# Kernel optimization log

Measured on AMD Instinct MI355X. Metric: run time of the kernel, lower is better.

Reference implementation:

```python
import jax, jax.numpy as jnp
import numpy as np

N, E, D_IN, L, H, U = 20000, 320000, 256, 4, 4, 64
HID = H * U  # 256
OUT = 64
LN_EPS = 1e-3  # keras LayerNormalization default epsilon
NEG_SLOPE = 0.2


def layer_norm(x, g, b):
    m = jnp.mean(x, axis=-1, keepdims=True)
    v = jnp.var(x, axis=-1, keepdims=True)
    return (x - m) * jax.lax.rsqrt(v + LN_EPS) * g + b


def gatv2(x, dst, src, Wl, Wr, a):
    # x: [N, HID]; Wl/Wr: [HID, H, U]; a: [H, U]
    zl = jnp.einsum('nd,dhu->nhu', x, Wl)  # target projection
    zr = jnp.einsum('nd,dhu->nhu', x, Wr)  # source projection / messages
    f = jax.nn.leaky_relu(zl[dst] + zr[src], NEG_SLOPE)       # [E, H, U]
    s = jnp.einsum('ehu,hu->eh', f, a)                        # [E, H]
    smax = jax.ops.segment_max(s, dst, num_segments=N)        # [N, H]
    es = jnp.exp(s - smax[dst])
    denom = jax.ops.segment_sum(es, dst, num_segments=N)      # [N, H]
    agg = jax.ops.segment_sum(es[:, :, None] * zr[src], dst, num_segments=N)
    agg = agg / (denom[:, :, None] + 1e-9)                    # [N, H, U]
    return agg.reshape(N, HID) + x  # residual (input dim == H*U)


def setup_inputs() -> dict:
    key = jax.random.key(0)
    ks = jax.random.split(key, 10)
    s_in = 1.0 / np.sqrt(D_IN)
    s_h = 1.0 / np.sqrt(HID)
    return {
        'x': jax.random.normal(ks[0], (N, D_IN), jnp.float32),
        'head_W': jax.random.normal(ks[1], (D_IN, HID), jnp.float32) * s_in,
        'head_b': jnp.zeros((HID,), jnp.float32),
        'ng_g': jnp.ones((L, HID), jnp.float32),
        'ng_b': jnp.zeros((L, HID), jnp.float32),
        'Wl': jax.random.normal(ks[2], (L, HID, H, U), jnp.float32) * s_h,
        'Wr': jax.random.normal(ks[3], (L, HID, H, U), jnp.float32) * s_h,
        'att': jax.random.normal(ks[4], (L, H, U), jnp.float32) * (1.0 / np.sqrt(U)),
        'nd_g': jnp.ones((L, HID), jnp.float32),
        'nd_b': jnp.zeros((L, HID), jnp.float32),
        'dense_W': jax.random.normal(ks[5], (L, HID, 4 * HID), jnp.float32) * s_h,
        'dense_b': jnp.zeros((L, 4 * HID), jnp.float32),
        'tail_W': jax.random.normal(ks[6], (HID, OUT), jnp.float32) * s_h,
        'tail_b': jnp.zeros((OUT,), jnp.float32),
        'edges': jax.random.randint(ks[7], (E, 2), 0, N, jnp.int32),
    }


def reference(x, head_W, head_b, ng_g, ng_b, Wl, Wr, att, nd_g, nd_b,
              dense_W, dense_b, tail_W, tail_b, edges):
    dst, src = edges[:, 0], edges[:, 1]
    h = x @ head_W + head_b  # head_layer
    for l in range(L):
        h = layer_norm(h, ng_g[l], ng_b[l])
        h = gatv2(h, dst, src, Wl[l], Wr[l], att[l])
        xr = layer_norm(h, nd_g[l], nd_b[l])
        # inference: dropout is identity
        d = jax.nn.gelu(xr @ dense_W[l] + dense_b[l], approximate=True)  # [N, 4*HID]
        h = d.reshape(N, 4, HID).sum(axis=1) + xr  # Add(split(.,4)) + residual
    return h @ tail_W + tail_b
```

## Files before the change

kernel.cpp:

```cpp
#include <hip/hip_runtime.h>
#include <cstdint>

#define NN 20000
#define EE 320000
#define DHID 256

typedef short bf16x8 __attribute__((ext_vector_type(8)));
typedef float f32x4 __attribute__((ext_vector_type(4)));


__device__ __forceinline__ float b2f(unsigned short u) {
    union { unsigned int i; float f; } v;
    v.i = ((unsigned int)u) << 16;
    return v.f;
}

__device__ __forceinline__ void b2f2(unsigned int w, float& lo, float& hi) {
    union { unsigned int i; float f; } a, c;
    a.i = w << 16;
    c.i = w & 0xffff0000u;
    lo = a.f;
    hi = c.f;
}

__device__ __forceinline__ unsigned short f2b(float x) {
    union { float f; unsigned int i; } v;
    v.f = x;
    unsigned int r = (v.i + 0x7FFFu + ((v.i >> 16) & 1u)) >> 16;
    return (unsigned short)r;
}

__device__ __forceinline__ float wave_sum(float v) {
#pragma unroll
    for (int m = 1; m < 64; m <<= 1) v += __shfl_xor(v, m);
    return v;
}

__device__ __forceinline__ float quad16_sum(float v) {
#pragma unroll
    for (int m = 1; m < 16; m <<= 1) v += __shfl_xor(v, m);
    return v;
}

__device__ __forceinline__ float gelu_f(float x) {
    float z = 0.7978845608028654f * (x + 0.044715f * x * x * x);
    float e = __expf(2.0f * z);
    float t = 1.0f - 2.0f / (e + 1.0f);
    return 0.5f * x * (1.0f + t);
}

__device__ __forceinline__ void gld16(const unsigned short* g, unsigned short* lds) {
    __builtin_amdgcn_global_load_lds((const __attribute__((address_space(1))) unsigned int*)g,
                                     (__attribute__((address_space(3))) unsigned int*)lds, 16, 0, 0);
}


__global__ void hist_kernel(const int* __restrict__ edges, int* __restrict__ counts, int E_) {
    int e = blockIdx.x * 256 + threadIdx.x;
    if (e >= E_) return;
    atomicAdd(&counts[edges[e * 2]], 1);
}

__global__ __launch_bounds__(1024) void scan_block(const int* __restrict__ counts,
                                                   int* __restrict__ excl,
                                                   int* __restrict__ bsums, int n) {
    __shared__ int sd[1024];
    int tid = threadIdx.x;
    int i = blockIdx.x * 1024 + tid;
    int c = (i < n) ? counts[i] : 0;
    sd[tid] = c;
    __syncthreads();
#pragma unroll
    for (int off = 1; off < 1024; off <<= 1) {
        int v = (tid >= off) ? sd[tid - off] : 0;
        __syncthreads();
        sd[tid] += v;
        __syncthreads();
    }
    if (i < n) excl[i] = sd[tid] - c;
    if (tid == 1023) bsums[blockIdx.x] = sd[1023];
}

__global__ void scan_tops(int* __restrict__ bsums, int nb) {
    if (threadIdx.x == 0 && blockIdx.x == 0) {
        int run = 0;
        for (int i = 0; i < nb; ++i) { int t = bsums[i]; bsums[i] = run; run += t; }
    }
}

__global__ void scan_fix(const int* __restrict__ excl, const int* __restrict__ bsums,
                         int* __restrict__ indptr, int* __restrict__ cursor, int n) {
    int i = blockIdx.x * 256 + threadIdx.x;
    if (i < n) {
        int v = excl[i] + bsums[i >> 10];
        indptr[i] = v;
        cursor[i] = v;
    }
    if (i == 0) indptr[n] = EE;
}

__global__ void scatter_kernel(const int* __restrict__ edges, int* __restrict__ cursor,
                               int* __restrict__ ssrc, int E_) {
    int e = blockIdx.x * 256 + threadIdx.x;
    if (e >= E_) return;
    int dstn = edges[e * 2];
    int src  = edges[e * 2 + 1];
    int pos = atomicAdd(&cursor[dstn], 1);
    ssrc[pos] = src;
}


__global__ __launch_bounds__(256) void transpose_bf16(const float* __restrict__ W,
                                                      unsigned short* __restrict__ Wt,
                                                      int K, int M, size_t lsW, size_t lsT) {
    W  += (size_t)blockIdx.z * lsW;
    Wt += (size_t)blockIdx.z * lsT;
    __shared__ float sm[32][33];
    int m0 = blockIdx.x * 32, k0 = blockIdx.y * 32;
    int tx = threadIdx.x & 31, ty = threadIdx.x >> 5;
#pragma unroll
    for (int i = 0; i < 4; ++i)
        sm[ty + i * 8][tx] = W[(size_t)(k0 + ty + i * 8) * M + m0 + tx];
    __syncthreads();
#pragma unroll
    for (int i = 0; i < 4; ++i)
        Wt[(size_t)(m0 + ty + i * 8) * K + k0 + tx] = f2b(sm[tx][ty + i * 8]);
}

__global__ void convert_bf16(const float* __restrict__ in, unsigned short* __restrict__ out, int n4) {
    int i = blockIdx.x * 256 + threadIdx.x;
    if (i >= n4) return;
    float4 v = *(const float4*)(in + (size_t)i * 4);
    ushort4 o;
    o.x = f2b(v.x); o.y = f2b(v.y); o.z = f2b(v.z); o.w = f2b(v.w);
    *(ushort4*)(out + (size_t)i * 4) = o;
}


__global__ __launch_bounds__(256) void ln_kernel(const float* __restrict__ X,
                                                 const float* __restrict__ g,
                                                 const float* __restrict__ b,
                                                 unsigned short* __restrict__ Yb, int nrows) {
    int row = blockIdx.x * 4 + (threadIdx.x >> 6);
    int lane = threadIdx.x & 63;
    if (row >= nrows) return;
    float4 v = *(const float4*)(X + (size_t)row * DHID + lane * 4);
    float sum = wave_sum(v.x + v.y + v.z + v.w);
    float sq  = wave_sum(v.x * v.x + v.y * v.y + v.z * v.z + v.w * v.w);
    float mean = sum * (1.0f / DHID);
    float var  = sq * (1.0f / DHID) - mean * mean;
    float r = rsqrtf(fmaxf(var, 0.0f) + 1e-3f);
    float4 gv = *(const float4*)(g + lane * 4);
    float4 bv = *(const float4*)(b + lane * 4);
    float4 o;
    o.x = (v.x - mean) * r * gv.x + bv.x;
    o.y = (v.y - mean) * r * gv.y + bv.y;
    o.z = (v.z - mean) * r * gv.z + bv.z;
    o.w = (v.w - mean) * r * gv.w + bv.w;
    ushort4 ob;
    ob.x = f2b(o.x); ob.y = f2b(o.y); ob.z = f2b(o.z); ob.w = f2b(o.w);
    *(ushort4*)(Yb + (size_t)row * DHID + lane * 4) = ob;
}

__global__ __launch_bounds__(256) void ln_dense(const unsigned short* __restrict__ d,
                                                const unsigned short* __restrict__ xrb,
                                                const float* __restrict__ g,
                                                const float* __restrict__ b,
                                                unsigned short* __restrict__ Yb, int nrows) {
    int row = blockIdx.x * 4 + (threadIdx.x >> 6);
    int lane = threadIdx.x & 63;
    if (row >= nrows) return;
    ushort4 xu = *(const ushort4*)(xrb + (size_t)row * DHID + lane * 4);
    float4 v;
    v.x = b2f(xu.x); v.y = b2f(xu.y); v.z = b2f(xu.z); v.w = b2f(xu.w);
#pragma unroll
    for (int c = 0; c < 4; ++c) {
        ushort4 t = *(const ushort4*)(d + (size_t)row * 1024 + c * 256 + lane * 4);
        v.x += b2f(t.x); v.y += b2f(t.y); v.z += b2f(t.z); v.w += b2f(t.w);
    }
    float sum = wave_sum(v.x + v.y + v.z + v.w);
    float sq  = wave_sum(v.x * v.x + v.y * v.y + v.z * v.z + v.w * v.w);
    float mean = sum * (1.0f / DHID);
    float var  = sq * (1.0f / DHID) - mean * mean;
    float r = rsqrtf(fmaxf(var, 0.0f) + 1e-3f);
    float4 gv = *(const float4*)(g + lane * 4);
    float4 bv = *(const float4*)(b + lane * 4);
    float4 o;
    o.x = (v.x - mean) * r * gv.x + bv.x;
    o.y = (v.y - mean) * r * gv.y + bv.y;
    o.z = (v.z - mean) * r * gv.z + bv.z;
    o.w = (v.w - mean) * r * gv.w + bv.w;
    ushort4 ob;
    ob.x = f2b(o.x); ob.y = f2b(o.y); ob.z = f2b(o.z); ob.w = f2b(o.w);
    *(ushort4*)(Yb + (size_t)row * DHID + lane * 4) = ob;
}

__global__ __launch_bounds__(256) void combine_final(const unsigned short* __restrict__ d,
                                                     const unsigned short* __restrict__ xrb,
                                                     unsigned short* __restrict__ hb, int nrows) {
    int row = blockIdx.x * 4 + (threadIdx.x >> 6);
    int lane = threadIdx.x & 63;
    if (row >= nrows) return;
    ushort4 xu = *(const ushort4*)(xrb + (size_t)row * DHID + lane * 4);
    float4 v;
    v.x = b2f(xu.x); v.y = b2f(xu.y); v.z = b2f(xu.z); v.w = b2f(xu.w);
#pragma unroll
    for (int c = 0; c < 4; ++c) {
        ushort4 t = *(const ushort4*)(d + (size_t)row * 1024 + c * 256 + lane * 4);
        v.x += b2f(t.x); v.y += b2f(t.y); v.z += b2f(t.z); v.w += b2f(t.w);
    }
    ushort4 ob;
    ob.x = f2b(v.x); ob.y = f2b(v.y); ob.z = f2b(v.z); ob.w = f2b(v.w);
    *(ushort4*)(hb + (size_t)row * DHID + lane * 4) = ob;
}


#define CS_STRIDE 140

template <int EP>
__global__ __launch_bounds__(256, 3) void gemm128(const unsigned short* __restrict__ A,
                                                  const unsigned short* __restrict__ B,
                                                  const float* __restrict__ bias,
                                                  void* __restrict__ Cv, int nrows, int ncols) {
    __shared__ unsigned short smem[128 * CS_STRIDE];
    unsigned short* As = smem;
    unsigned short* Bs = smem + 8192;
    unsigned short* Cs = smem;
    const int bm = blockIdx.x * 128, bn = blockIdx.y * 128;
    if (bm >= nrows) return;
    const int tid  = threadIdx.x;
    const int w    = tid >> 6, lane = tid & 63;
    const int quad = lane >> 4, l16 = lane & 15;
    const int wm = w >> 1, wn = w & 1;

    const int srow = lane & 15;
    const int sg   = lane >> 4;
    int ga0 = min(bm + w * 32 + srow,      nrows - 1);
    int ga1 = min(bm + w * 32 + 16 + srow, nrows - 1);
    int gb0 = min(bn + w * 32 + srow,      ncols - 1);
    int gb1 = min(bn + w * 32 + 16 + srow, ncols - 1);
    const unsigned short* Ap0 = A + (size_t)ga0 * 256 + sg * 8;
    const unsigned short* Ap1 = A + (size_t)ga1 * 256 + sg * 8;
    const unsigned short* Bp0 = B + (size_t)gb0 * 256 + sg * 8;
    const unsigned short* Bp1 = B + (size_t)gb1 * 256 + sg * 8;
    unsigned short* la0 = As + (2 * w) * 1024;
    unsigned short* la1 = As + (2 * w + 1) * 1024;
    unsigned short* lb0 = Bs + (2 * w) * 1024;
    unsigned short* lb1 = Bs + (2 * w + 1) * 1024;

    f32x4 acc[4][4] = {};
    for (int k0 = 0; k0 < 256; k0 += 64) {
        gld16(Ap0 + k0,      la0);
        gld16(Ap0 + k0 + 32, la0 + 512);
        gld16(Ap1 + k0,      la1);
        gld16(Ap1 + k0 + 32, la1 + 512);
        gld16(Bp0 + k0,      lb0);
        gld16(Bp0 + k0 + 32, lb0 + 512);
        gld16(Bp1 + k0,      lb1);
        gld16(Bp1 + k0 + 32, lb1 + 512);
        __syncthreads();
#pragma unroll
        for (int kk = 0; kk < 2; ++kk) {
            bf16x8 a[4], b[4];
#pragma unroll
            for (int mi = 0; mi < 4; ++mi)
                a[mi] = *(const bf16x8*)(As + (wm * 4 + mi) * 1024 + (kk * 4 + quad) * 128 + l16 * 8);
#pragma unroll
            for (int ni = 0; ni < 4; ++ni)
                b[ni] = *(const bf16x8*)(Bs + (wn * 4 + ni) * 1024 + (kk * 4 + quad) * 128 + l16 * 8);
#pragma unroll
            for (int mi = 0; mi < 4; ++mi)
#pragma unroll
                for (int ni = 0; ni < 4; ++ni)
                    acc[mi][ni] = __builtin_amdgcn_mfma_f32_16x16x32_bf16(a[mi], b[ni], acc[mi][ni], 0, 0, 0);
        }
        __syncthreads();
    }

    if (EP == 0) {
#pragma unroll
        for (int ni = 0; ni < 4; ++ni) {
            int col = bn + wn * 64 + ni * 16 + l16;
            if (col >= ncols) continue;
            float bv = bias ? bias[col] : 0.0f;
#pragma unroll
            for (int mi = 0; mi < 4; ++mi) {
#pragma unroll
                for (int r = 0; r < 4; ++r) {
                    int row = bm + wm * 64 + mi * 16 + quad * 4 + r;
                    if (row < nrows) ((float*)Cv)[(size_t)row * ncols + col] = acc[mi][ni][r] + bv;
                }
            }
        }
    } else {
#pragma unroll
        for (int ni = 0; ni < 4; ++ni) {
            int lc = wn * 64 + ni * 16 + l16;
            float bv = (EP == 2) ? bias[bn + lc] : 0.0f;
#pragma unroll
            for (int mi = 0; mi < 4; ++mi) {
#pragma unroll
                for (int r = 0; r < 4; ++r) {
                    int lr = wm * 64 + mi * 16 + quad * 4 + r;
                    float v = acc[mi][ni][r] + bv;
                    Cs[lr * CS_STRIDE + lc] = f2b(EP == 2 ? gelu_f(v) : v);
                }
            }
        }
        __syncthreads();
#pragma unroll
        for (int i = 0; i < 8; ++i) {
            int id = tid + 256 * i;
            int lr = id >> 4;
            int lc = (id & 15) * 8;
            int grow = bm + lr;
            if (grow < nrows) {
                uint4 val = *(const uint4*)(Cs + lr * CS_STRIDE + lc);
                *(uint4*)((unsigned short*)Cv + (size_t)grow * ncols + bn + lc) = val;
            }
        }
    }
}


__global__ __launch_bounds__(256) void gat_fused(const unsigned short* __restrict__ zb,
                                                 const float* __restrict__ att,
                                                 const int* __restrict__ ssrc,
                                                 const int* __restrict__ indptr,
                                                 const unsigned short* __restrict__ hnb,
                                                 const float* __restrict__ g,
                                                 const float* __restrict__ b,
                                                 unsigned short* __restrict__ xrb, int nrows) {
    int wid = threadIdx.x >> 6;
    int lane = threadIdx.x & 63;
    int n = blockIdx.x * 4 + wid;
    if (n >= nrows) return;
    int start = indptr[n];
    int end = indptr[n + 1];

    ushort4 zlu = *(const ushort4*)(zb + (size_t)n * 512 + lane * 4);
    float zl0 = b2f(zlu.x), zl1 = b2f(zlu.y), zl2 = b2f(zlu.z), zl3 = b2f(zlu.w);
    float4 a4 = *(const float4*)(att + lane * 4);
    size_t idx = (size_t)n * DHID + lane * 4;
    ushort4 ru = *(const ushort4*)(hnb + idx);
    float rr0 = b2f(ru.x), rr1 = b2f(ru.y), rr2 = b2f(ru.z), rr3 = b2f(ru.w);

    float denom = 0.f;
    float ax = 0.f, ay = 0.f, az = 0.f, aw = 0.f;

    const uint2* zrp = (const uint2*)(zb + 256);
    uint2 c0 = make_uint2(0, 0), c1 = make_uint2(0, 0);
    uint2 c2 = make_uint2(0, 0), c3 = make_uint2(0, 0);
    uint2 c4 = make_uint2(0, 0), c5 = make_uint2(0, 0);
    uint2 c6 = make_uint2(0, 0), c7 = make_uint2(0, 0);
    if (start < end) {
        int e1 = end - 1;
        c0 = zrp[(size_t)ssrc[start] * 128 + lane];
        c1 = zrp[(size_t)ssrc[min(start + 1, e1)] * 128 + lane];
        c2 = zrp[(size_t)ssrc[min(start + 2, e1)] * 128 + lane];
        c3 = zrp[(size_t)ssrc[min(start + 3, e1)] * 128 + lane];
        c4 = zrp[(size_t)ssrc[min(start + 4, e1)] * 128 + lane];
        c5 = zrp[(size_t)ssrc[min(start + 5, e1)] * 128 + lane];
        c6 = zrp[(size_t)ssrc[min(start + 6, e1)] * 128 + lane];
        c7 = zrp[(size_t)ssrc[min(start + 7, e1)] * 128 + lane];
    }
    for (int p = start; p < end; p += 4) {
        uint2 u0 = c0, u1 = c1, u2 = c2, u3 = c3;
        c0 = c4; c1 = c5; c2 = c6; c3 = c7;
        if (p + 8 < end) {
            int e1 = end - 1;
            c4 = zrp[(size_t)ssrc[p + 8] * 128 + lane];
            c5 = zrp[(size_t)ssrc[min(p + 9,  e1)] * 128 + lane];
            c6 = zrp[(size_t)ssrc[min(p + 10, e1)] * 128 + lane];
            c7 = zrp[(size_t)ssrc[min(p + 11, e1)] * 128 + lane];
        }
        float z00, z01, z02, z03, z10, z11, z12, z13;
        float z20, z21, z22, z23, z30, z31, z32, z33;
        b2f2(u0.x, z00, z01); b2f2(u0.y, z02, z03);
        b2f2(u1.x, z10, z11); b2f2(u1.y, z12, z13);
        b2f2(u2.x, z20, z21); b2f2(u2.y, z22, z23);
        b2f2(u3.x, z30, z31); b2f2(u3.y, z32, z33);

        float v00 = zl0 + z00, v01 = zl1 + z01, v02 = zl2 + z02, v03 = zl3 + z03;
        float v10 = zl0 + z10, v11 = zl1 + z11, v12 = zl2 + z12, v13 = zl3 + z13;
        float v20 = zl0 + z20, v21 = zl1 + z21, v22 = zl2 + z22, v23 = zl3 + z23;
        float v30 = zl0 + z30, v31 = zl1 + z31, v32 = zl2 + z32, v33 = zl3 + z33;
        v00 = (v00 > 0.f) ? v00 : 0.2f * v00;
        v01 = (v01 > 0.f) ? v01 : 0.2f * v01;
        v02 = (v02 > 0.f) ? v02 : 0.2f * v02;
        v03 = (v03 > 0.f) ? v03 : 0.2f * v03;
        v10 = (v10 > 0.f) ? v10 : 0.2f * v10;
        v11 = (v11 > 0.f) ? v11 : 0.2f * v11;
        v12 = (v12 > 0.f) ? v12 : 0.2f * v12;
        v13 = (v13 > 0.f) ? v13 : 0.2f * v13;
        v20 = (v20 > 0.f) ? v20 : 0.2f * v20;
        v21 = (v21 > 0.f) ? v21 : 0.2f * v21;
        v22 = (v22 > 0.f) ? v22 : 0.2f * v22;
        v23 = (v23 > 0.f) ? v23 : 0.2f * v23;
        v30 = (v30 > 0.f) ? v30 : 0.2f * v30;
        v31 = (v31 > 0.f) ? v31 : 0.2f * v31;
        v32 = (v32 > 0.f) ? v32 : 0.2f * v32;
        v33 = (v33 > 0.f) ? v33 : 0.2f * v33;
        float p0 = a4.x * v00 + a4.y * v01 + a4.z * v02 + a4.w * v03;
        float p1 = a4.x * v10 + a4.y * v11 + a4.z * v12 + a4.w * v13;
        float p2 = a4.x * v20 + a4.y * v21 + a4.z * v22 + a4.w * v23;
        float p3 = a4.x * v30 + a4.y * v31 + a4.z * v32 + a4.w * v33;
        float s0 = quad16_sum(p0);
        float s1 = quad16_sum(p1);
        float s2 = quad16_sum(p2);
        float s3 = quad16_sum(p3);
        bool b1 = (p + 1 < end), b2 = (p + 2 < end), b3 = (p + 3 < end);
        float w0 = __expf(s0);
        float w1 = b1 ? __expf(s1) : 0.0f;
        float w2 = b2 ? __expf(s2) : 0.0f;
        float w3 = b3 ? __expf(s3) : 0.0f;
        denom += (w0 + w1) + (w2 + w3);
        ax += (w0 * z00 + w1 * z10) + (w2 * z20 + w3 * z30);
        ay += (w0 * z01 + w1 * z11) + (w2 * z21 + w3 * z31);
        az += (w0 * z02 + w1 * z12) + (w2 * z22 + w3 * z32);
        aw += (w0 * z03 + w1 * z13) + (w2 * z23 + w3 * z33);
    }
    float inv = 1.0f / (denom + 1e-9f);
    float4 o;
    o.x = ax * inv + rr0;
    o.y = ay * inv + rr1;
    o.z = az * inv + rr2;
    o.w = aw * inv + rr3;
    float sum = wave_sum(o.x + o.y + o.z + o.w);
    float sq  = wave_sum(o.x * o.x + o.y * o.y + o.z * o.z + o.w * o.w);
    float mean = sum * (1.0f / DHID);
    float var  = sq * (1.0f / DHID) - mean * mean;
    float rnorm = rsqrtf(fmaxf(var, 0.0f) + 1e-3f);
    float4 gv = *(const float4*)(g + lane * 4);
    float4 bv = *(const float4*)(b + lane * 4);
    float4 y;
    y.x = (o.x - mean) * rnorm * gv.x + bv.x;
    y.y = (o.y - mean) * rnorm * gv.y + bv.y;
    y.z = (o.z - mean) * rnorm * gv.z + bv.z;
    y.w = (o.w - mean) * rnorm * gv.w + bv.w;
    ushort4 ob;
    ob.x = f2b(y.x); ob.y = f2b(y.y); ob.z = f2b(y.z); ob.w = f2b(y.w);
    *(ushort4*)(xrb + idx) = ob;
}


extern "C" void kernel_launch(void* const* d_in, const int* in_sizes, int n_in,
                              void* d_out, int out_size, void* d_ws, size_t ws_size,
                              hipStream_t stream) {
    const float* x       = (const float*)d_in[0];
    const float* head_W  = (const float*)d_in[1];
    const float* head_b  = (const float*)d_in[2];
    const float* ng_g    = (const float*)d_in[3];
    const float* ng_b    = (const float*)d_in[4];
    const float* Wl      = (const float*)d_in[5];
    const float* Wr      = (const float*)d_in[6];
    const float* att     = (const float*)d_in[7];
    const float* nd_g    = (const float*)d_in[8];
    const float* nd_b    = (const float*)d_in[9];
    const float* dense_W = (const float*)d_in[10];
    const float* dense_b = (const float*)d_in[11];
    const float* tail_W  = (const float*)d_in[12];
    const float* tail_b  = (const float*)d_in[13];
    const int*   edges   = (const int*)d_in[14];
    float* out = (float*)d_out;

    const size_t NH = (size_t)NN * DHID;
    float* xr = (float*)d_ws;
    float* hn = xr + NH;
    unsigned short* hnb = (unsigned short*)(hn + NH);
    unsigned short* xrb = hnb + NH;
    unsigned short* U   = xrb + NH;
    unsigned short* zb  = U;
    unsigned short* d_buf = U;
    unsigned short* headT  = U + 4 * NH;
    unsigned short* WzT    = headT + 65536;
    unsigned short* denseT = WzT + 524288;
    unsigned short* tailT  = denseT + 1048576;
    int* counts = (int*)(tailT + 16384);
    int* bsums  = counts + NN;
    int* excl   = bsums + 32;
    int* indptr = excl + NN;
    int* cursor = indptr + NN + 1;
    int* ssrc   = cursor + NN;

    hipMemsetAsync(counts, 0, NN * sizeof(int), stream);
    hist_kernel<<<(EE + 255) / 256, 256, 0, stream>>>(edges, counts, EE);
    scan_block<<<(NN + 1023) / 1024, 1024, 0, stream>>>(counts, excl, bsums, NN);
    scan_tops<<<1, 64, 0, stream>>>(bsums, (NN + 1023) / 1024);
    scan_fix<<<(NN + 255) / 256, 256, 0, stream>>>(excl, bsums, indptr, cursor, NN);
    scatter_kernel<<<(EE + 255) / 256, 256, 0, stream>>>(edges, cursor, ssrc, EE);

    transpose_bf16<<<dim3(8, 8, 1), 256, 0, stream>>>(head_W, headT, 256, 256, 0, 0);
    transpose_bf16<<<dim3(8, 8, 4), 256, 0, stream>>>(Wl, WzT, 256, 256, 65536, 131072);
    transpose_bf16<<<dim3(8, 8, 4), 256, 0, stream>>>(Wr, WzT + 65536, 256, 256, 65536, 131072);
    transpose_bf16<<<dim3(32, 8, 4), 256, 0, stream>>>(dense_W, denseT, 256, 1024, 262144, 262144);
    transpose_bf16<<<dim3(2, 8, 1), 256, 0, stream>>>(tail_W, tailT, 256, 64, 0, 0);
    convert_bf16<<<(int)(NH / 4 + 255) / 256, 256, 0, stream>>>(x, hnb, (int)(NH / 4));

    const int GXP = 160;
    gemm128<0><<<dim3(GXP, 2), 256, 0, stream>>>(hnb, headT, head_b, xr, NN, 256);

    for (int l = 0; l < 4; ++l) {
        if (l == 0)
            ln_kernel<<<NN / 4, 256, 0, stream>>>(xr, ng_g, ng_b, hnb, NN);
        else
            ln_dense<<<NN / 4, 256, 0, stream>>>(d_buf, xrb, ng_g + l * 256, ng_b + l * 256, hnb, NN);
        gemm128<1><<<dim3(GXP, 4), 256, 0, stream>>>(hnb, WzT + (size_t)l * 131072, nullptr, zb, NN, 512);
        gat_fused<<<(NN + 3) / 4, 256, 0, stream>>>(zb, att + l * 256, ssrc, indptr, hnb,
                                                    nd_g + l * 256, nd_b + l * 256, xrb, NN);
        gemm128<2><<<dim3(GXP, 8), 256, 0, stream>>>(xrb, denseT + (size_t)l * 262144,
                                                     dense_b + l * 1024, d_buf, NN, 1024);
    }
    combine_final<<<NN / 4, 256, 0, stream>>>(d_buf, xrb, hnb, NN);
    gemm128<0><<<dim3(GXP, 1), 256, 0, stream>>>(hnb, tailT, tail_b, out, NN, 64);
}
```

Measured before the change: 585.4 us.

## Reduce dense GELU chunks in GEMM epilogue and sort GAT nodes by degree

The dense weight is transposed with a permuted column order so that the four chunks summed by split-add land in adjacent columns. The GEMM epilogue applies GELU and then sums groups of four with lane shuffles, writing a 256-wide output instead of 1024 and removing the 4x reread in the LN/combine kernels. GAT nodes are processed in degree-sorted order for wave load balance, gathers use scalar indices via readfirstlane, and a zero-padded ssrc tail removes the min clamps. LeakyReLU becomes fmax. The changes also move ssrc into the hn buffer and sum the bf16 GELU outputs in fp32 before rounding.

```diff
diff --git a/kernel.cpp b/kernel.cpp
--- a/kernel.cpp
+++ b/kernel.cpp
@@ -110,6 +110,28 @@
 }
 
 
+__global__ void deg_hist(const int* __restrict__ counts, int* __restrict__ dh, int n) {
+    int i = blockIdx.x * 256 + threadIdx.x;
+    if (i < n) atomicAdd(&dh[min(counts[i], 63)], 1);
+}
+
+__global__ void deg_scan(int* __restrict__ dh) {
+    if (threadIdx.x == 0 && blockIdx.x == 0) {
+        int run = 0;
+        for (int i = 0; i < 64; ++i) { int t = dh[i]; dh[i] = run; run += t; }
+    }
+}
+
+__global__ void deg_scatter(const int* __restrict__ counts, int* __restrict__ dh,
+                            int* __restrict__ norder, int n) {
+    int i = blockIdx.x * 256 + threadIdx.x;
+    if (i < n) {
+        int pos = atomicAdd(&dh[min(counts[i], 63)], 1);
+        norder[pos] = i;
+    }
+}
+
+
 __global__ __launch_bounds__(256) void transpose_bf16(const float* __restrict__ W,
                                                       unsigned short* __restrict__ Wt,
                                                       int K, int M, size_t lsW, size_t lsT) {
@@ -125,6 +147,26 @@
 #pragma unroll
     for (int i = 0; i < 4; ++i)
         Wt[(size_t)(m0 + ty + i * 8) * K + k0 + tx] = f2b(sm[tx][ty + i * 8]);
+}
+
+__global__ __launch_bounds__(256) void transpose_perm(const float* __restrict__ W,
+                                                      unsigned short* __restrict__ Wt,
+                                                      int K, int M, size_t lsW, size_t lsT) {
+    W  += (size_t)blockIdx.z * lsW;
+    Wt += (size_t)blockIdx.z * lsT;
+    __shared__ float sm[32][33];
+    int m0 = blockIdx.x * 32, k0 = blockIdx.y * 32;
+    int tx = threadIdx.x & 31, ty = threadIdx.x >> 5;
+#pragma unroll
+    for (int i = 0; i < 4; ++i)
+        sm[ty + i * 8][tx] = W[(size_t)(k0 + ty + i * 8) * M + m0 + tx];
+    __syncthreads();
+#pragma unroll
+    for (int i = 0; i < 4; ++i) {
+        int mm = m0 + ty + i * 8;
+        int cc = ((mm & 255) << 2) | (mm >> 8);
+        Wt[(size_t)cc * K + k0 + tx] = f2b(sm[tx][ty + i * 8]);
+    }
 }
 
 __global__ void convert_bf16(const float* __restrict__ in, unsigned short* __restrict__ out, int n4) {
@@ -171,13 +213,12 @@
     int lane = threadIdx.x & 63;
     if (row >= nrows) return;
     ushort4 xu = *(const ushort4*)(xrb + (size_t)row * DHID + lane * 4);
+    ushort4 du = *(const ushort4*)(d   + (size_t)row * DHID + lane * 4);
     float4 v;
-    v.x = b2f(xu.x); v.y = b2f(xu.y); v.z = b2f(xu.z); v.w = b2f(xu.w);
-#pragma unroll
-    for (int c = 0; c < 4; ++c) {
-        ushort4 t = *(const ushort4*)(d + (size_t)row * 1024 + c * 256 + lane * 4);
-        v.x += b2f(t.x); v.y += b2f(t.y); v.z += b2f(t.z); v.w += b2f(t.w);
-    }
+    v.x = b2f(xu.x) + b2f(du.x);
+    v.y = b2f(xu.y) + b2f(du.y);
+    v.z = b2f(xu.z) + b2f(du.z);
+    v.w = b2f(xu.w) + b2f(du.w);
     float sum = wave_sum(v.x + v.y + v.z + v.w);
     float sq  = wave_sum(v.x * v.x + v.y * v.y + v.z * v.z + v.w * v.w);
     float mean = sum * (1.0f / DHID);
@@ -202,20 +243,18 @@
     int lane = threadIdx.x & 63;
     if (row >= nrows) return;
     ushort4 xu = *(const ushort4*)(xrb + (size_t)row * DHID + lane * 4);
-    float4 v;
-    v.x = b2f(xu.x); v.y = b2f(xu.y); v.z = b2f(xu.z); v.w = b2f(xu.w);
-#pragma unroll
-    for (int c = 0; c < 4; ++c) {
-        ushort4 t = *(const ushort4*)(d + (size_t)row * 1024 + c * 256 + lane * 4);
-        v.x += b2f(t.x); v.y += b2f(t.y); v.z += b2f(t.z); v.w += b2f(t.w);
-    }
+    ushort4 du = *(const ushort4*)(d   + (size_t)row * DHID + lane * 4);
     ushort4 ob;
-    ob.x = f2b(v.x); ob.y = f2b(v.y); ob.z = f2b(v.z); ob.w = f2b(v.w);
+    ob.x = f2b(b2f(xu.x) + b2f(du.x));
+    ob.y = f2b(b2f(xu.y) + b2f(du.y));
+    ob.z = f2b(b2f(xu.z) + b2f(du.z));
+    ob.w = f2b(b2f(xu.w) + b2f(du.w));
     *(ushort4*)(hb + (size_t)row * DHID + lane * 4) = ob;
 }
 
 
 #define CS_STRIDE 140
+#define CS2_STRIDE 40
 
 template <int EP>
 __global__ __launch_bounds__(256, 3) void gemm128(const unsigned short* __restrict__ A,
@@ -292,18 +331,16 @@
                 }
             }
         }
-    } else {
+    } else if (EP == 1) {
 #pragma unroll
         for (int ni = 0; ni < 4; ++ni) {
             int lc = wn * 64 + ni * 16 + l16;
-            float bv = (EP == 2) ? bias[bn + lc] : 0.0f;
 #pragma unroll
             for (int mi = 0; mi < 4; ++mi) {
 #pragma unroll
                 for (int r = 0; r < 4; ++r) {
                     int lr = wm * 64 + mi * 16 + quad * 4 + r;
-                    float v = acc[mi][ni][r] + bv;
-                    Cs[lr * CS_STRIDE + lc] = f2b(EP == 2 ? gelu_f(v) : v);
+                    Cs[lr * CS_STRIDE + lc] = f2b(acc[mi][ni][r]);
                 }
             }
         }
@@ -319,6 +356,40 @@
                 *(uint4*)((unsigned short*)Cv + (size_t)grow * ncols + bn + lc) = val;
             }
         }
+    } else {
+        unsigned short* Cs2 = smem;
+#pragma unroll
+        for (int ni = 0; ni < 4; ++ni) {
+            int lc = wn * 64 + ni * 16 + l16;
+            int cc = bn + lc;
+            int oc = ((cc & 3) << 8) | (cc >> 2);
+            float bv = bias[oc];
+#pragma unroll
+            for (int mi = 0; mi < 4; ++mi) {
+#pragma unroll
+                for (int r = 0; r < 4; ++r) {
+                    float v = gelu_f(acc[mi][ni][r] + bv);
+                    v += __shfl_xor(v, 1);
+                    v += __shfl_xor(v, 2);
+                    if ((l16 & 3) == 0) {
+                        int lr = wm * 64 + mi * 16 + quad * 4 + r;
+                        Cs2[lr * CS2_STRIDE + (lc >> 2)] = f2b(v);
+                    }
+                }
+            }
+        }
+        __syncthreads();
+#pragma unroll
+        for (int i = 0; i < 2; ++i) {
+            int id = tid + 256 * i;
+            int lr = id >> 2;
+            int q  = id & 3;
+            int grow = bm + lr;
+            if (grow < nrows) {
+                uint4 val = *(const uint4*)(Cs2 + lr * CS2_STRIDE + q * 8);
+                *(uint4*)((unsigned short*)Cv + (size_t)grow * 256 + (bn >> 2) + q * 8) = val;
+            }
+        }
     }
 }
 
@@ -327,16 +398,18 @@
                                                  const float* __restrict__ att,
                                                  const int* __restrict__ ssrc,
                                                  const int* __restrict__ indptr,
+                                                 const int* __restrict__ norder,
                                                  const unsigned short* __restrict__ hnb,
                                                  const float* __restrict__ g,
                                                  const float* __restrict__ b,
                                                  unsigned short* __restrict__ xrb, int nrows) {
     int wid = threadIdx.x >> 6;
     int lane = threadIdx.x & 63;
-    int n = blockIdx.x * 4 + wid;
-    if (n >= nrows) return;
-    int start = indptr[n];
-    int end = indptr[n + 1];
+    int n0 = blockIdx.x * 4 + wid;
+    if (n0 >= nrows) return;
+    int n     = __builtin_amdgcn_readfirstlane(norder[n0]);
+    int start = __builtin_amdgcn_readfirstlane(indptr[n]);
+    int end   = __builtin_amdgcn_readfirstlane(indptr[n + 1]);
 
     ushort4 zlu = *(const ushort4*)(zb + (size_t)n * 512 + lane * 4);
     float zl0 = b2f(zlu.x), zl1 = b2f(zlu.y), zl2 = b2f(zlu.z), zl3 = b2f(zlu.w);
@@ -348,31 +421,29 @@
     float denom = 0.f;
     float ax = 0.f, ay = 0.f, az = 0.f, aw = 0.f;
 
-    const uint2* zrp = (const uint2*)(zb + 256);
-    uint2 c0 = make_uint2(0, 0), c1 = make_uint2(0, 0);
-    uint2 c2 = make_uint2(0, 0), c3 = make_uint2(0, 0);
-    uint2 c4 = make_uint2(0, 0), c5 = make_uint2(0, 0);
-    uint2 c6 = make_uint2(0, 0), c7 = make_uint2(0, 0);
-    if (start < end) {
-        int e1 = end - 1;
-        c0 = zrp[(size_t)ssrc[start] * 128 + lane];
-        c1 = zrp[(size_t)ssrc[min(start + 1, e1)] * 128 + lane];
-        c2 = zrp[(size_t)ssrc[min(start + 2, e1)] * 128 + lane];
-        c3 = zrp[(size_t)ssrc[min(start + 3, e1)] * 128 + lane];
-        c4 = zrp[(size_t)ssrc[min(start + 4, e1)] * 128 + lane];
-        c5 = zrp[(size_t)ssrc[min(start + 5, e1)] * 128 + lane];
-        c6 = zrp[(size_t)ssrc[min(start + 6, e1)] * 128 + lane];
-        c7 = zrp[(size_t)ssrc[min(start + 7, e1)] * 128 + lane];
-    }
+    const char* zrbase = (const char*)(zb + 256) + (size_t)lane * 8;
+    auto GATHER = [&](int e) -> uint2 {
+        int sv = __builtin_amdgcn_readfirstlane(ssrc[e]);
+        return *(const uint2*)(zrbase + ((size_t)sv << 10));
+    };
+
+    uint2 c0 = GATHER(start);
+    uint2 c1 = GATHER(start + 1);
+    uint2 c2 = GATHER(start + 2);
+    uint2 c3 = GATHER(start + 3);
+    uint2 c4 = GATHER(start + 4);
+    uint2 c5 = GATHER(start + 5);
+    uint2 c6 = GATHER(start + 6);
+    uint2 c7 = GATHER(start + 7);
+
     for (int p = start; p < end; p += 4) {
         uint2 u0 = c0, u1 = c1, u2 = c2, u3 = c3;
         c0 = c4; c1 = c5; c2 = c6; c3 = c7;
         if (p + 8 < end) {
-            int e1 = end - 1;
-            c4 = zrp[(size_t)ssrc[p + 8] * 128 + lane];
-            c5 = zrp[(size_t)ssrc[min(p + 9,  e1)] * 128 + lane];
-            c6 = zrp[(size_t)ssrc[min(p + 10, e1)] * 128 + lane];
-            c7 = zrp[(size_t)ssrc[min(p + 11, e1)] * 128 + lane];
+            c4 = GATHER(p + 8);
+            c5 = GATHER(p + 9);
+            c6 = GATHER(p + 10);
+            c7 = GATHER(p + 11);
         }
         float z00, z01, z02, z03, z10, z11, z12, z13;
         float z20, z21, z22, z23, z30, z31, z32, z33;
@@ -385,22 +456,14 @@
         float v10 = zl0 + z10, v11 = zl1 + z11, v12 = zl2 + z12, v13 = zl3 + z13;
         float v20 = zl0 + z20, v21 = zl1 + z21, v22 = zl2 + z22, v23 = zl3 + z23;
         float v30 = zl0 + z30, v31 = zl1 + z31, v32 = zl2 + z32, v33 = zl3 + z33;
-        v00 = (v00 > 0.f) ? v00 : 0.2f * v00;
-        v01 = (v01 > 0.f) ? v01 : 0.2f * v01;
-        v02 = (v02 > 0.f) ? v02 : 0.2f * v02;
-        v03 = (v03 > 0.f) ? v03 : 0.2f * v03;
-        v10 = (v10 > 0.f) ? v10 : 0.2f * v10;
-        v11 = (v11 > 0.f) ? v11 : 0.2f * v11;
-        v12 = (v12 > 0.f) ? v12 : 0.2f * v12;
-        v13 = (v13 > 0.f) ? v13 : 0.2f * v13;
-        v20 = (v20 > 0.f) ? v20 : 0.2f * v20;
-        v21 = (v21 > 0.f) ? v21 : 0.2f * v21;
-        v22 = (v22 > 0.f) ? v22 : 0.2f * v22;
-        v23 = (v23 > 0.f) ? v23 : 0.2f * v23;
-        v30 = (v30 > 0.f) ? v30 : 0.2f * v30;
-        v31 = (v31 > 0.f) ? v31 : 0.2f * v31;
-        v32 = (v32 > 0.f) ? v32 : 0.2f * v32;
-        v33 = (v33 > 0.f) ? v33 : 0.2f * v33;
+        v00 = fmaxf(v00, 0.2f * v00); v01 = fmaxf(v01, 0.2f * v01);
+        v02 = fmaxf(v02, 0.2f * v02); v03 = fmaxf(v03, 0.2f * v03);
+        v10 = fmaxf(v10, 0.2f * v10); v11 = fmaxf(v11, 0.2f * v11);
+        v12 = fmaxf(v12, 0.2f * v12); v13 = fmaxf(v13, 0.2f * v13);
+        v20 = fmaxf(v20, 0.2f * v20); v21 = fmaxf(v21, 0.2f * v21);
+        v22 = fmaxf(v22, 0.2f * v22); v23 = fmaxf(v23, 0.2f * v23);
+        v30 = fmaxf(v30, 0.2f * v30); v31 = fmaxf(v31, 0.2f * v31);
+        v32 = fmaxf(v32, 0.2f * v32); v33 = fmaxf(v33, 0.2f * v33);
         float p0 = a4.x * v00 + a4.y * v01 + a4.z * v02 + a4.w * v03;
         float p1 = a4.x * v10 + a4.y * v11 + a4.z * v12 + a4.w * v13;
         float p2 = a4.x * v20 + a4.y * v21 + a4.z * v22 + a4.w * v23;
@@ -481,10 +544,17 @@
     int* excl   = bsums + 32;
     int* indptr = excl + NN;
     int* cursor = indptr + NN + 1;
-    int* ssrc   = cursor + NN;
+    int* ssrc   = (int*)hn;
+    int* norder = ssrc + EE + 16;
+    int* dh     = norder + NN;
 
     hipMemsetAsync(counts, 0, NN * sizeof(int), stream);
+    hipMemsetAsync(dh, 0, 64 * sizeof(int), stream);
+    hipMemsetAsync(ssrc + EE, 0, 16 * sizeof(int), stream);
     hist_kernel<<<(EE + 255) / 256, 256, 0, stream>>>(edges, counts, EE);
+    deg_hist<<<(NN + 255) / 256, 256, 0, stream>>>(counts, dh, NN);
+    deg_scan<<<1, 64, 0, stream>>>(dh);
+    deg_scatter<<<(NN + 255) / 256, 256, 0, stream>>>(counts, dh, norder, NN);
     scan_block<<<(NN + 1023) / 1024, 1024, 0, stream>>>(counts, excl, bsums, NN);
     scan_tops<<<1, 64, 0, stream>>>(bsums, (NN + 1023) / 1024);
     scan_fix<<<(NN + 255) / 256, 256, 0, stream>>>(excl, bsums, indptr, cursor, NN);
@@ -493,7 +563,7 @@
     transpose_bf16<<<dim3(8, 8, 1), 256, 0, stream>>>(head_W, headT, 256, 256, 0, 0);
     transpose_bf16<<<dim3(8, 8, 4), 256, 0, stream>>>(Wl, WzT, 256, 256, 65536, 131072);
     transpose_bf16<<<dim3(8, 8, 4), 256, 0, stream>>>(Wr, WzT + 65536, 256, 256, 65536, 131072);
-    transpose_bf16<<<dim3(32, 8, 4), 256, 0, stream>>>(dense_W, denseT, 256, 1024, 262144, 262144);
+    transpose_perm<<<dim3(32, 8, 4), 256, 0, stream>>>(dense_W, denseT, 256, 1024, 262144, 262144);
     transpose_bf16<<<dim3(2, 8, 1), 256, 0, stream>>>(tail_W, tailT, 256, 64, 0, 0);
     convert_bf16<<<(int)(NH / 4 + 255) / 256, 256, 0, stream>>>(x, hnb, (int)(NH / 4));
 
@@ -506,9 +576,9 @@
         else
             ln_dense<<<NN / 4, 256, 0, stream>>>(d_buf, xrb, ng_g + l * 256, ng_b + l * 256, hnb, NN);
         gemm128<1><<<dim3(GXP, 4), 256, 0, stream>>>(hnb, WzT + (size_t)l * 131072, nullptr, zb, NN, 512);
-        gat_fused<<<(NN + 3) / 4, 256, 0, stream>>>(zb, att + l * 256, ssrc, indptr, hnb,
+        gat_fused<<<(NN + 3) / 4, 256, 0, stream>>>(zb, att + l * 256, ssrc, indptr, norder, hnb,
                                                     nd_g + l * 256, nd_b + l * 256, xrb, NN);
-        gemm128<2><<<dim3(GXP, 8), 256, 0, stream>>>(xrb, denseT + (size_t)l * 262144,
+        gemm128<3><<<dim3(GXP, 8), 256, 0, stream>>>(xrb, denseT + (size_t)l * 262144,
                                                      dense_b + l * 1024, d_buf, NN, 1024);
     }
     combine_final<<<NN / 4, 256, 0, stream>>>(d_buf, xrb, hnb, NN);
```

Measured after the change: 671.2 us. +14.7%, slower.

## Fuse split-sum of GELU dense output into GEMM epilogue via column permutation

Applied to the files above, without the earlier changes.

Permutes the dense weight columns so that each 128-column GEMM tile holds the four split chunks for 32 output features. The epilogue then sums the four GELU results in registers and writes a 256-wide output instead of 1024-wide, and ln_dense and combine_final now read a single chunk. This cuts the write and reread of the intermediate d buffer by about four times. It also replaces the leaky-ReLU selects in the GAT kernel with fmaxf. The permutation index math must match the MFMA fragment layout exactly, so a mismatch would silently give wrong results.

```diff
diff --git a/kernel.cpp b/kernel.cpp
--- a/kernel.cpp
+++ b/kernel.cpp
@@ -125,6 +125,28 @@
 #pragma unroll
     for (int i = 0; i < 4; ++i)
         Wt[(size_t)(m0 + ty + i * 8) * K + k0 + tx] = f2b(sm[tx][ty + i * 8]);
+}
+
+__global__ __launch_bounds__(256) void transpose_perm(const float* __restrict__ W,
+                                                      unsigned short* __restrict__ Wt,
+                                                      int K, int M, size_t lsW, size_t lsT) {
+    W  += (size_t)blockIdx.z * lsW;
+    Wt += (size_t)blockIdx.z * lsT;
+    __shared__ float sm[32][33];
+    int m0 = blockIdx.x * 32, k0 = blockIdx.y * 32;
+    int tx = threadIdx.x & 31, ty = threadIdx.x >> 5;
+#pragma unroll
+    for (int i = 0; i < 4; ++i)
+        sm[ty + i * 8][tx] = W[(size_t)(k0 + ty + i * 8) * M + m0 + tx];
+    __syncthreads();
+#pragma unroll
+    for (int i = 0; i < 4; ++i) {
+        int mm = m0 + ty + i * 8;
+        int c = mm >> 8, j = mm & 255;
+        int by = j >> 5, t = j & 31;
+        int cc = (by << 7) | ((t >> 4) << 6) | (c << 4) | (t & 15);
+        Wt[(size_t)cc * K + k0 + tx] = f2b(sm[tx][ty + i * 8]);
+    }
 }
 
 __global__ void convert_bf16(const float* __restrict__ in, unsigned short* __restrict__ out, int n4) {
@@ -171,13 +193,12 @@
     int lane = threadIdx.x & 63;
     if (row >= nrows) return;
     ushort4 xu = *(const ushort4*)(xrb + (size_t)row * DHID + lane * 4);
+    ushort4 du = *(const ushort4*)(d   + (size_t)row * DHID + lane * 4);
     float4 v;
-    v.x = b2f(xu.x); v.y = b2f(xu.y); v.z = b2f(xu.z); v.w = b2f(xu.w);
-#pragma unroll
-    for (int c = 0; c < 4; ++c) {
-        ushort4 t = *(const ushort4*)(d + (size_t)row * 1024 + c * 256 + lane * 4);
-        v.x += b2f(t.x); v.y += b2f(t.y); v.z += b2f(t.z); v.w += b2f(t.w);
-    }
+    v.x = b2f(xu.x) + b2f(du.x);
+    v.y = b2f(xu.y) + b2f(du.y);
+    v.z = b2f(xu.z) + b2f(du.z);
+    v.w = b2f(xu.w) + b2f(du.w);
     float sum = wave_sum(v.x + v.y + v.z + v.w);
     float sq  = wave_sum(v.x * v.x + v.y * v.y + v.z * v.z + v.w * v.w);
     float mean = sum * (1.0f / DHID);
@@ -202,20 +223,18 @@
     int lane = threadIdx.x & 63;
     if (row >= nrows) return;
     ushort4 xu = *(const ushort4*)(xrb + (size_t)row * DHID + lane * 4);
-    float4 v;
-    v.x = b2f(xu.x); v.y = b2f(xu.y); v.z = b2f(xu.z); v.w = b2f(xu.w);
-#pragma unroll
-    for (int c = 0; c < 4; ++c) {
-        ushort4 t = *(const ushort4*)(d + (size_t)row * 1024 + c * 256 + lane * 4);
-        v.x += b2f(t.x); v.y += b2f(t.y); v.z += b2f(t.z); v.w += b2f(t.w);
-    }
+    ushort4 du = *(const ushort4*)(d   + (size_t)row * DHID + lane * 4);
     ushort4 ob;
-    ob.x = f2b(v.x); ob.y = f2b(v.y); ob.z = f2b(v.z); ob.w = f2b(v.w);
+    ob.x = f2b(b2f(xu.x) + b2f(du.x));
+    ob.y = f2b(b2f(xu.y) + b2f(du.y));
+    ob.z = f2b(b2f(xu.z) + b2f(du.z));
+    ob.w = f2b(b2f(xu.w) + b2f(du.w));
     *(ushort4*)(hb + (size_t)row * DHID + lane * 4) = ob;
 }
 
 
 #define CS_STRIDE 140
+#define CS2_STRIDE 40
 
 template <int EP>
 __global__ __launch_bounds__(256, 3) void gemm128(const unsigned short* __restrict__ A,
@@ -292,18 +311,16 @@
                 }
             }
         }
-    } else {
+    } else if (EP == 1) {
 #pragma unroll
         for (int ni = 0; ni < 4; ++ni) {
             int lc = wn * 64 + ni * 16 + l16;
-            float bv = (EP == 2) ? bias[bn + lc] : 0.0f;
 #pragma unroll
             for (int mi = 0; mi < 4; ++mi) {
 #pragma unroll
                 for (int r = 0; r < 4; ++r) {
                     int lr = wm * 64 + mi * 16 + quad * 4 + r;
-                    float v = acc[mi][ni][r] + bv;
-                    Cs[lr * CS_STRIDE + lc] = f2b(EP == 2 ? gelu_f(v) : v);
+                    Cs[lr * CS_STRIDE + lc] = f2b(acc[mi][ni][r]);
                 }
             }
         }
@@ -317,6 +334,36 @@
             if (grow < nrows) {
                 uint4 val = *(const uint4*)(Cs + lr * CS_STRIDE + lc);
                 *(uint4*)((unsigned short*)Cv + (size_t)grow * ncols + bn + lc) = val;
+            }
+        }
+    } else {
+        unsigned short* Cs2 = smem;
+        int jfl = wn * 16 + l16;
+        int jf  = (bn >> 2) + jfl;
+        float bv0 = bias[jf];
+        float bv1 = bias[256 + jf];
+        float bv2 = bias[512 + jf];
+        float bv3 = bias[768 + jf];
+#pragma unroll
+        for (int mi = 0; mi < 4; ++mi) {
+#pragma unroll
+            for (int r = 0; r < 4; ++r) {
+                float v = gelu_f(acc[mi][0][r] + bv0) + gelu_f(acc[mi][1][r] + bv1)
+                        + gelu_f(acc[mi][2][r] + bv2) + gelu_f(acc[mi][3][r] + bv3);
+                int lr = wm * 64 + mi * 16 + quad * 4 + r;
+                Cs2[lr * CS2_STRIDE + jfl] = f2b(v);
+            }
+        }
+        __syncthreads();
+#pragma unroll
+        for (int i = 0; i < 2; ++i) {
+            int id = tid + 256 * i;
+            int lr = id >> 2;
+            int q  = id & 3;
+            int grow = bm + lr;
+            if (grow < nrows) {
+                uint4 val = *(const uint4*)(Cs2 + lr * CS2_STRIDE + q * 8);
+                *(uint4*)((unsigned short*)Cv + (size_t)grow * 256 + (bn >> 2) + q * 8) = val;
             }
         }
     }
@@ -385,22 +432,14 @@
         float v10 = zl0 + z10, v11 = zl1 + z11, v12 = zl2 + z12, v13 = zl3 + z13;
         float v20 = zl0 + z20, v21 = zl1 + z21, v22 = zl2 + z22, v23 = zl3 + z23;
         float v30 = zl0 + z30, v31 = zl1 + z31, v32 = zl2 + z32, v33 = zl3 + z33;
-        v00 = (v00 > 0.f) ? v00 : 0.2f * v00;
-        v01 = (v01 > 0.f) ? v01 : 0.2f * v01;
-        v02 = (v02 > 0.f) ? v02 : 0.2f * v02;
-        v03 = (v03 > 0.f) ? v03 : 0.2f * v03;
-        v10 = (v10 > 0.f) ? v10 : 0.2f * v10;
-        v11 = (v11 > 0.f) ? v11 : 0.2f * v11;
-        v12 = (v12 > 0.f) ? v12 : 0.2f * v12;
-        v13 = (v13 > 0.f) ? v13 : 0.2f * v13;
-        v20 = (v20 > 0.f) ? v20 : 0.2f * v20;
-        v21 = (v21 > 0.f) ? v21 : 0.2f * v21;
-        v22 = (v22 > 0.f) ? v22 : 0.2f * v22;
-        v23 = (v23 > 0.f) ? v23 : 0.2f * v23;
-        v30 = (v30 > 0.f) ? v30 : 0.2f * v30;
-        v31 = (v31 > 0.f) ? v31 : 0.2f * v31;
-        v32 = (v32 > 0.f) ? v32 : 0.2f * v32;
-        v33 = (v33 > 0.f) ? v33 : 0.2f * v33;
+        v00 = fmaxf(v00, 0.2f * v00); v01 = fmaxf(v01, 0.2f * v01);
+        v02 = fmaxf(v02, 0.2f * v02); v03 = fmaxf(v03, 0.2f * v03);
+        v10 = fmaxf(v10, 0.2f * v10); v11 = fmaxf(v11, 0.2f * v11);
+        v12 = fmaxf(v12, 0.2f * v12); v13 = fmaxf(v13, 0.2f * v13);
+        v20 = fmaxf(v20, 0.2f * v20); v21 = fmaxf(v21, 0.2f * v21);
+        v22 = fmaxf(v22, 0.2f * v22); v23 = fmaxf(v23, 0.2f * v23);
+        v30 = fmaxf(v30, 0.2f * v30); v31 = fmaxf(v31, 0.2f * v31);
+        v32 = fmaxf(v32, 0.2f * v32); v33 = fmaxf(v33, 0.2f * v33);
         float p0 = a4.x * v00 + a4.y * v01 + a4.z * v02 + a4.w * v03;
         float p1 = a4.x * v10 + a4.y * v11 + a4.z * v12 + a4.w * v13;
         float p2 = a4.x * v20 + a4.y * v21 + a4.z * v22 + a4.w * v23;
@@ -493,7 +532,7 @@
     transpose_bf16<<<dim3(8, 8, 1), 256, 0, stream>>>(head_W, headT, 256, 256, 0, 0);
     transpose_bf16<<<dim3(8, 8, 4), 256, 0, stream>>>(Wl, WzT, 256, 256, 65536, 131072);
     transpose_bf16<<<dim3(8, 8, 4), 256, 0, stream>>>(Wr, WzT + 65536, 256, 256, 65536, 131072);
-    transpose_bf16<<<dim3(32, 8, 4), 256, 0, stream>>>(dense_W, denseT, 256, 1024, 262144, 262144);
+    transpose_perm<<<dim3(32, 8, 4), 256, 0, stream>>>(dense_W, denseT, 256, 1024, 262144, 262144);
     transpose_bf16<<<dim3(2, 8, 1), 256, 0, stream>>>(tail_W, tailT, 256, 64, 0, 0);
     convert_bf16<<<(int)(NH / 4 + 255) / 256, 256, 0, stream>>>(x, hnb, (int)(NH / 4));
 
@@ -508,7 +547,7 @@
         gemm128<1><<<dim3(GXP, 4), 256, 0, stream>>>(hnb, WzT + (size_t)l * 131072, nullptr, zb, NN, 512);
         gat_fused<<<(NN + 3) / 4, 256, 0, stream>>>(zb, att + l * 256, ssrc, indptr, hnb,
                                                     nd_g + l * 256, nd_b + l * 256, xrb, NN);
-        gemm128<2><<<dim3(GXP, 8), 256, 0, stream>>>(xrb, denseT + (size_t)l * 262144,
+        gemm128<3><<<dim3(GXP, 8), 256, 0, stream>>>(xrb, denseT + (size_t)l * 262144,
                                                      dense_b + l * 1024, d_buf, NN, 1024);
     }
     combine_final<<<NN / 4, 256, 0, stream>>>(d_buf, xrb, hnb, NN);
```

Measured after the change: 552.7 us. 1.06x faster.
